# Performance work log

Hardware: AMD Instinct MI355X
Metric: run time of the kernel (lower is better)

Reference implementation:

```python
import jax, jax.numpy as jnp
import numpy as np
import math

D = 1024
H = 16
DH = D // H
FF = 4096
B, S = 2, 2048


def _layernorm(x, g, b, eps=1e-5):
    mu = jnp.mean(x, axis=-1, keepdims=True)
    var = jnp.var(x, axis=-1, keepdims=True)
    return (x - mu) * jax.lax.rsqrt(var + eps) * g + b


def _gelu_tanh(x):
    # 0.5*x*(1+tanh(sqrt(2/pi)*(x+0.044715*x^3)))
    c = math.sqrt(2.0 / math.pi)
    return 0.5 * x * (1.0 + jnp.tanh(c * (x + 0.044715 * x ** 3)))


def setup_inputs() -> dict:
    key = jax.random.key(0)
    ks = jax.random.split(key, 8)
    s = 0.02
    return {
        "x": jax.random.normal(ks[0], (B, S, D), dtype=jnp.float32),
        "ln1_g": jnp.ones((D,), jnp.float32),
        "ln1_b": jnp.zeros((D,), jnp.float32),
        "Wqkv": jax.random.normal(ks[1], (D, 3 * D), jnp.float32) * s,
        "bqkv": jnp.zeros((3 * D,), jnp.float32),
        "Wo": jax.random.normal(ks[2], (D, D), jnp.float32) * s,
        "bo": jnp.zeros((D,), jnp.float32),
        "ln2_g": jnp.ones((D,), jnp.float32),
        "ln2_b": jnp.zeros((D,), jnp.float32),
        "W1": jax.random.normal(ks[3], (D, FF), jnp.float32) * s,
        "b1": jnp.zeros((FF,), jnp.float32),
        "W2": jax.random.normal(ks[4], (FF, D), jnp.float32) * s,
        "b2": jnp.zeros((D,), jnp.float32),
    }


def reference(x, ln1_g, ln1_b, Wqkv, bqkv, Wo, bo, ln2_g, ln2_b, W1, b1, W2, b2):
    b, s, d = x.shape
    h = _layernorm(x, ln1_g, ln1_b)
    qkv = h @ Wqkv + bqkv                       # [B,S,3D]
    q, k, v = jnp.split(qkv, 3, axis=-1)
    q = q.reshape(b, s, H, DH).transpose(0, 2, 1, 3)   # [B,H,S,Dh]
    k = k.reshape(b, s, H, DH).transpose(0, 2, 1, 3)
    v = v.reshape(b, s, H, DH).transpose(0, 2, 1, 3)
    scores = jnp.einsum("bhqd,bhkd->bhqk", q, k) / math.sqrt(DH)
    probs = jax.nn.softmax(scores, axis=-1)
    attn = jnp.einsum("bhqk,bhkd->bhqd", probs, v)     # [B,H,S,Dh]
    attn = attn.transpose(0, 2, 1, 3).reshape(b, s, d)
    attn = attn @ Wo + bo
    x = x + attn
    m = _layernorm(x, ln2_g, ln2_b)
    m = _gelu_tanh(m @ W1 + b1) @ W2 + b2
    return x + m
```

## Files before the change

kernel.cpp:

```cpp
#include <hip/hip_runtime.h>
#include <hip/hip_bf16.h>
#include <cstdint>

#define D_ 1024
#define H_ 16
#define DH_ 64
#define FF_ 4096
#define B_ 2
#define S_ 2048
#define MR_ (B_ * S_)

typedef __bf16 bf16x8 __attribute__((ext_vector_type(8)));
typedef __bf16 bf16x4 __attribute__((ext_vector_type(4)));
typedef float f32x4 __attribute__((ext_vector_type(4)));
typedef float f32x16 __attribute__((ext_vector_type(16)));

__device__ __forceinline__ void g2lds16(const void* g, void* l) {
  __builtin_amdgcn_global_load_lds(
      (__attribute__((address_space(1))) void*)(uintptr_t)g,
      (__attribute__((address_space(3))) void*)(uint32_t)(uintptr_t)l,
      16, 0, 0);
}

__device__ __forceinline__ unsigned pkbf16(float lo, float hi) {
  unsigned r;
  asm("v_cvt_pk_bf16_f32 %0, %1, %2" : "=v"(r) : "v"(lo), "v"(hi));
  return r;
}

__device__ __forceinline__ float fexp2(float x) {
  return __builtin_amdgcn_exp2f(x);
}

__global__ __launch_bounds__(256) void transpose_cvt(
    const float* __restrict__ W, __hip_bfloat16* __restrict__ Wt, int K, int N) {
  __shared__ float t[32][33];
  int bx = blockIdx.x * 32;
  int by = blockIdx.y * 32;
  int tx = threadIdx.x, ty = threadIdx.y;
#pragma unroll
  for (int i = 0; i < 4; ++i)
    t[ty + 8 * i][tx] = W[(size_t)(by + ty + 8 * i) * N + bx + tx];
  __syncthreads();
#pragma unroll
  for (int i = 0; i < 4; ++i)
    Wt[(size_t)(bx + ty + 8 * i) * K + by + tx] = __float2bfloat16(t[tx][ty + 8 * i]);
}

__global__ __launch_bounds__(256) void transpose_v(
    const __hip_bfloat16* __restrict__ qkv, __hip_bfloat16* __restrict__ vT) {
  __shared__ __hip_bfloat16 t[32][33];
  int bh = blockIdx.z, b = bh >> 4, h = bh & 15;
  int s0 = blockIdx.x * 32, d0 = blockIdx.y * 32;
  int tx = threadIdx.x, ty = threadIdx.y;
#pragma unroll
  for (int i = 0; i < 4; ++i)
    t[ty + 8 * i][tx] =
        qkv[(size_t)(b * S_ + s0 + ty + 8 * i) * (3 * D_) + 2 * D_ + h * DH_ + d0 + tx];
  __syncthreads();
#pragma unroll
  for (int i = 0; i < 4; ++i)
    vT[(size_t)(bh * DH_ + d0 + ty + 8 * i) * S_ + s0 + tx] = t[tx][ty + 8 * i];
}

__global__ __launch_bounds__(256) void ln_kernel(
    const float* __restrict__ x, const float* __restrict__ g,
    const float* __restrict__ b, __hip_bfloat16* __restrict__ out) {
  int row = blockIdx.x;
  const float4* xr = (const float4*)(x + (size_t)row * D_);
  float4 v = xr[threadIdx.x];
  float s = v.x + v.y + v.z + v.w;
  float ss = v.x * v.x + v.y * v.y + v.z * v.z + v.w * v.w;
#pragma unroll
  for (int m = 1; m < 64; m <<= 1) {
    s += __shfl_xor(s, m);
    ss += __shfl_xor(ss, m);
  }
  __shared__ float rs[4], rss[4];
  int wave = threadIdx.x >> 6, lane = threadIdx.x & 63;
  if (lane == 0) { rs[wave] = s; rss[wave] = ss; }
  __syncthreads();
  s = rs[0] + rs[1] + rs[2] + rs[3];
  ss = rss[0] + rss[1] + rss[2] + rss[3];
  float mean = s * (1.0f / D_);
  float var = ss * (1.0f / D_) - mean * mean;
  float inv = rsqrtf(var + 1e-5f);
  int c = threadIdx.x * 4;
  float4 gv = ((const float4*)g)[threadIdx.x];
  float4 bv = ((const float4*)b)[threadIdx.x];
  __hip_bfloat16* o = out + (size_t)row * D_ + c;
  o[0] = __float2bfloat16((v.x - mean) * inv * gv.x + bv.x);
  o[1] = __float2bfloat16((v.y - mean) * inv * gv.y + bv.y);
  o[2] = __float2bfloat16((v.z - mean) * inv * gv.z + bv.z);
  o[3] = __float2bfloat16((v.w - mean) * inv * gv.w + bv.w);
}

template <int EPI>
__global__ __launch_bounds__(256) void gemm4(
    const __hip_bfloat16* __restrict__ A, const __hip_bfloat16* __restrict__ Bt,
    const float* __restrict__ bias, const float* __restrict__ resid,
    void* __restrict__ outp, int M, int N, int K) {
  constexpr int BM = 128, BN = 128, MF = 4, NF = 4;
  __shared__ alignas(16) __hip_bfloat16 sA[2][BM * 64];
  __shared__ alignas(16) __hip_bfloat16 sB[2][BN * 64];
  const int tid = threadIdx.x;
  const int lane = tid & 63, wave = tid >> 6;
  const int l15 = lane & 15, l4 = lane >> 4;
  const int wr = wave >> 1, wc = wave & 1;
  const int csw = (l15 & 7) << 3;

  const int gx = gridDim.x;
  int nwg = gx * gridDim.y;
  int flat = blockIdx.y * gx + blockIdx.x;
  int cpx = nwg >> 3;
  int swz = (flat & 7) * cpx + (flat >> 3);
  const int m0 = (swz / gx) * BM, n0 = (swz % gx) * BN;

  f32x4 z = {0.f, 0.f, 0.f, 0.f};
  f32x4 acc[MF][NF];
#pragma unroll
  for (int i = 0; i < MF; ++i)
#pragma unroll
    for (int j = 0; j < NF; ++j) acc[i][j] = z;

  auto stage = [&](int bu, int kt) {
#pragma unroll
    for (int it = 0; it < 4; ++it) {
      int idx = it * 256 + tid;
      int r = idx >> 3, c = (idx & 7) * 8;
      int cs = c ^ ((r & 7) << 3);
      g2lds16(A + (size_t)(m0 + r) * K + kt + cs, (void*)(&sA[bu][idx * 8]));
      g2lds16(Bt + (size_t)(n0 + r) * K + kt + cs, (void*)(&sB[bu][idx * 8]));
    }
  };

  const int nk = K / 64;
  stage(0, 0);
  asm volatile("s_waitcnt vmcnt(0)" ::: "memory");
  __builtin_amdgcn_s_barrier();

  for (int j = 0; j < nk; ++j) {
    const int cur = j & 1;
    if (j + 1 < nk) stage(cur ^ 1, (j + 1) * 64);

    __builtin_amdgcn_s_setprio(1);
#pragma unroll
    for (int kk = 0; kk < 2; ++kk) {
      int col = (kk * 32 + l4 * 8) ^ csw;
      bf16x8 bfr[NF];
#pragma unroll
      for (int nf = 0; nf < NF; ++nf)
        bfr[nf] = *(const bf16x8*)(&sB[cur][(wc * 64 + nf * 16 + l15) * 64 + col]);
#pragma unroll
      for (int mf = 0; mf < MF; ++mf) {
        bf16x8 af = *(const bf16x8*)(&sA[cur][(wr * 64 + mf * 16 + l15) * 64 + col]);
#pragma unroll
        for (int nf = 0; nf < NF; ++nf)
          acc[mf][nf] =
              __builtin_amdgcn_mfma_f32_16x16x32_bf16(af, bfr[nf], acc[mf][nf], 0, 0, 0);
      }
    }
    __builtin_amdgcn_s_setprio(0);

    asm volatile("s_waitcnt lgkmcnt(0)" ::: "memory");
    __builtin_amdgcn_sched_barrier(0);
    asm volatile("s_waitcnt vmcnt(0)" ::: "memory");
    __builtin_amdgcn_s_barrier();
    asm volatile("" ::: "memory");
  }

#pragma unroll
  for (int mf = 0; mf < MF; ++mf) {
#pragma unroll
    for (int nf = 0; nf < NF; ++nf) {
      int col = n0 + wc * 64 + nf * 16 + l15;
      float bv = bias[col];
#pragma unroll
      for (int j = 0; j < 4; ++j) {
        int row = m0 + wr * 64 + mf * 16 + l4 * 4 + j;
        size_t o = (size_t)row * N + col;
        float v = acc[mf][nf][j] + bv;
        if (EPI == 0) {
          ((__hip_bfloat16*)outp)[o] = __float2bfloat16(v);
        } else if (EPI == 1) {
          ((float*)outp)[o] = v + resid[o];
        } else {
          float a = 0.7978845608028654f * (v + 0.044715f * v * v * v);
          a = fminf(fmaxf(a, -15.f), 15.f);
          float e = __expf(2.f * a);
          float th = (e - 1.f) / (e + 1.f);
          ((__hip_bfloat16*)outp)[o] = __float2bfloat16(0.5f * v * (1.f + th));
        }
      }
    }
  }
}

template <int EPI>
__global__ __launch_bounds__(512) void gemmr3(
    const __hip_bfloat16* __restrict__ A, const __hip_bfloat16* __restrict__ Bt,
    const float* __restrict__ bias, const float* __restrict__ resid,
    void* __restrict__ outp, int M, int N, int K) {
  constexpr int BM = 128, BN = 128, MF = 4, NF = 2, WN = 4;
  __shared__ alignas(16) __hip_bfloat16 sA[3][BM * 64];
  __shared__ alignas(16) __hip_bfloat16 sB[3][BN * 64];
  const int tid = threadIdx.x;
  const int lane = tid & 63, wave = tid >> 6;
  const int l15 = lane & 15, l4 = lane >> 4;
  const int wr = wave / WN, wc = wave % WN;
  const int csw = (l15 & 7) << 3;

  const int gx = gridDim.x;
  int nwg = gx * gridDim.y;
  int flat = blockIdx.y * gx + blockIdx.x;
  int cpx = nwg >> 3;
  int swz = (flat & 7) * cpx + (flat >> 3);
  const int m0 = (swz / gx) * BM, n0 = (swz % gx) * BN;

  f32x4 z = {0.f, 0.f, 0.f, 0.f};
  f32x4 acc[MF][NF];
#pragma unroll
  for (int i = 0; i < MF; ++i)
#pragma unroll
    for (int j = 0; j < NF; ++j) acc[i][j] = z;

  auto stage = [&](int bu, int kt) {
#pragma unroll
    for (int it = 0; it < 2; ++it) {
      int idx = it * 512 + tid;
      int r = idx >> 3, c = (idx & 7) * 8;
      int cs = c ^ ((r & 7) << 3);
      g2lds16(A + (size_t)(m0 + r) * K + kt + cs, (void*)(&sA[bu][idx * 8]));
      g2lds16(Bt + (size_t)(n0 + r) * K + kt + cs, (void*)(&sB[bu][idx * 8]));
    }
  };

  const int nk = K / 64;
  stage(0, 0);
  stage(1, 64);
  asm volatile("s_waitcnt vmcnt(4)" ::: "memory");
  __builtin_amdgcn_s_barrier();

  int bu = 0, bu2 = 2;
  for (int j = 0; j < nk; ++j) {
    const bool pf = (j + 2) < nk;
    if (pf) stage(bu2, (j + 2) * 64);

    __builtin_amdgcn_s_setprio(1);
#pragma unroll
    for (int kk = 0; kk < 2; ++kk) {
      int col = (kk * 32 + l4 * 8) ^ csw;
      bf16x8 bfr[NF];
#pragma unroll
      for (int nf = 0; nf < NF; ++nf)
        bfr[nf] = *(const bf16x8*)(&sB[bu][(wc * NF * 16 + nf * 16 + l15) * 64 + col]);
#pragma unroll
      for (int mf = 0; mf < MF; ++mf) {
        bf16x8 af = *(const bf16x8*)(&sA[bu][(wr * MF * 16 + mf * 16 + l15) * 64 + col]);
#pragma unroll
        for (int nf = 0; nf < NF; ++nf)
          acc[mf][nf] =
              __builtin_amdgcn_mfma_f32_16x16x32_bf16(af, bfr[nf], acc[mf][nf], 0, 0, 0);
      }
    }
    __builtin_amdgcn_s_setprio(0);

    asm volatile("s_waitcnt lgkmcnt(0)" ::: "memory");
    __builtin_amdgcn_sched_barrier(0);
    if (pf)
      asm volatile("s_waitcnt vmcnt(4)" ::: "memory");
    else
      asm volatile("s_waitcnt vmcnt(0)" ::: "memory");
    __builtin_amdgcn_s_barrier();
    asm volatile("" ::: "memory");
    bu = (bu == 2) ? 0 : bu + 1;
    bu2 = (bu2 == 2) ? 0 : bu2 + 1;
  }

#pragma unroll
  for (int mf = 0; mf < MF; ++mf) {
#pragma unroll
    for (int nf = 0; nf < NF; ++nf) {
      int col = n0 + wc * NF * 16 + nf * 16 + l15;
      float bv = bias[col];
#pragma unroll
      for (int j = 0; j < 4; ++j) {
        int row = m0 + wr * MF * 16 + mf * 16 + l4 * 4 + j;
        size_t o = (size_t)row * N + col;
        float v = acc[mf][nf][j] + bv;
        if (EPI == 0) {
          ((__hip_bfloat16*)outp)[o] = __float2bfloat16(v);
        } else if (EPI == 1) {
          ((float*)outp)[o] = v + resid[o];
        } else {
          float a = 0.7978845608028654f * (v + 0.044715f * v * v * v);
          a = fminf(fmaxf(a, -15.f), 15.f);
          float e = __expf(2.f * a);
          float th = (e - 1.f) / (e + 1.f);
          ((__hip_bfloat16*)outp)[o] = __float2bfloat16(0.5f * v * (1.f + th));
        }
      }
    }
  }
}

__global__ __launch_bounds__(256) void attn_kernel(
    const __hip_bfloat16* __restrict__ qkv, const __hip_bfloat16* __restrict__ vT,
    __hip_bfloat16* __restrict__ out) {
  __shared__ alignas(16) __hip_bfloat16 sK[2][64 * 64];
  __shared__ alignas(16) __hip_bfloat16 sV[2][64 * 64];
  const int tid = threadIdx.x, lane = tid & 63, wave = tid >> 6;
  const int l31 = lane & 31, hi = lane >> 5;
  const int bh = blockIdx.y, b = bh >> 4, h = bh & 15;
  const int q0 = blockIdx.x * 128;
  const int rsw = (l31 & 7) << 3;
  const float k2 = 0.125f * 1.44269504f;

  bf16x8 qf[4];
  {
    int qr = q0 + wave * 32 + l31;
    const size_t qbase = ((size_t)(b * S_ + qr)) * (3 * D_) + h * DH_;
#pragma unroll
    for (int ks = 0; ks < 4; ++ks) {
      bf16x8 q = *(const bf16x8*)(qkv + qbase + ks * 16 + hi * 8);
#pragma unroll
      for (int i = 0; i < 8; ++i) q[i] = (__bf16)((float)q[i] * k2);
      qf[ks] = q;
    }
  }

  bf16x8 onesb;
#pragma unroll
  for (int i = 0; i < 8; ++i) onesb[i] = (__bf16)1.0f;

  f32x16 acc0, acc1, accL;
#pragma unroll
  for (int r = 0; r < 16; ++r) { acc0[r] = 0.f; acc1[r] = 0.f; accL[r] = 0.f; }

  const __hip_bfloat16* kg = qkv + (size_t)b * S_ * (3 * D_) + D_ + h * DH_;
  const __hip_bfloat16* vg = vT + (size_t)bh * DH_ * S_;

  auto stage = [&](int bu, int kv0) {
#pragma unroll
    for (int it = 0; it < 2; ++it) {
      int idx = it * 256 + tid;
      int r = idx >> 3;
      int c = (idx & 7) * 8;
      int cs = c ^ ((r & 7) << 3);
      g2lds16(kg + (size_t)(kv0 + r) * (3 * D_) + cs, (void*)(&sK[bu][idx * 8]));
      g2lds16(vg + (size_t)r * S_ + kv0 + cs, (void*)(&sV[bu][idx * 8]));
    }
  };

  stage(0, 0);
  const int NT = S_ / 64;

  for (int t = 0; t < NT; ++t) {
    const int cur = t & 1;
    __syncthreads();
    if (t + 1 < NT) stage(cur ^ 1, (t + 1) * 64);

    f32x16 sf0, sf1;
#pragma unroll
    for (int r = 0; r < 16; ++r) { sf0[r] = 0.f; sf1[r] = 0.f; }
    __builtin_amdgcn_s_setprio(1);
#pragma unroll
    for (int ks = 0; ks < 4; ++ks) {
      int colsw = (ks * 16 + hi * 8) ^ rsw;
      bf16x8 kf0 = *(const bf16x8*)(&sK[cur][l31 * 64 + colsw]);
      bf16x8 kf1 = *(const bf16x8*)(&sK[cur][(32 + l31) * 64 + colsw]);
      sf0 = __builtin_amdgcn_mfma_f32_32x32x16_bf16(kf0, qf[ks], sf0, 0, 0, 0);
      sf1 = __builtin_amdgcn_mfma_f32_32x32x16_bf16(kf1, qf[ks], sf1, 0, 0, 0);
    }
    __builtin_amdgcn_s_setprio(0);

    bf16x8 pa[4];
#pragma unroll
    for (int kb = 0; kb < 2; ++kb) {
      const f32x16 s16 = kb ? sf1 : sf0;
#pragma unroll
      for (int ksb = 0; ksb < 2; ++ksb) {
        float p0 = fexp2(s16[8 * ksb + 0]);
        float p1 = fexp2(s16[8 * ksb + 1]);
        float p2 = fexp2(s16[8 * ksb + 2]);
        float p3 = fexp2(s16[8 * ksb + 3]);
        float p4 = fexp2(s16[8 * ksb + 4]);
        float p5 = fexp2(s16[8 * ksb + 5]);
        float p6 = fexp2(s16[8 * ksb + 6]);
        float p7 = fexp2(s16[8 * ksb + 7]);
        unsigned wa = pkbf16(p0, p1), wb = pkbf16(p2, p3);
        unsigned wc = pkbf16(p4, p5), wd = pkbf16(p6, p7);
        auto r1 = __builtin_amdgcn_permlane32_swap(wa, wc, false, false);
        auto r2 = __builtin_amdgcn_permlane32_swap(wb, wd, false, false);
        union { unsigned u[4]; bf16x8 v; } w;
        w.u[0] = r1[0]; w.u[1] = r2[0]; w.u[2] = r1[1]; w.u[3] = r2[1];
        pa[kb * 2 + ksb] = w.v;
      }
    }

    __builtin_amdgcn_s_setprio(1);
#pragma unroll
    for (int ksg = 0; ksg < 4; ++ksg) {
      int colsw = (ksg * 16 + hi * 8) ^ rsw;
      bf16x8 vf0 = *(const bf16x8*)(&sV[cur][l31 * 64 + colsw]);
      bf16x8 vf1 = *(const bf16x8*)(&sV[cur][(32 + l31) * 64 + colsw]);
      acc0 = __builtin_amdgcn_mfma_f32_32x32x16_bf16(pa[ksg], vf0, acc0, 0, 0, 0);
      acc1 = __builtin_amdgcn_mfma_f32_32x32x16_bf16(pa[ksg], vf1, acc1, 0, 0, 0);
      accL = __builtin_amdgcn_mfma_f32_32x32x16_bf16(pa[ksg], onesb, accL, 0, 0, 0);
    }
    __builtin_amdgcn_s_setprio(0);
  }

#pragma unroll
  for (int r = 0; r < 16; ++r) {
    int qrow = (r & 3) + 8 * (r >> 2) + 4 * hi;
    float ir = 1.0f / accL[r];
    size_t obase = ((size_t)(b * S_ + q0 + wave * 32 + qrow)) * D_ + h * DH_ + l31;
    out[obase] = __float2bfloat16(acc0[r] * ir);
    out[obase + 32] = __float2bfloat16(acc1[r] * ir);
  }
}

extern "C" void kernel_launch(void* const* d_in, const int* in_sizes, int n_in,
                              void* d_out, int out_size, void* d_ws, size_t ws_size,
                              hipStream_t stream) {
  const float* x = (const float*)d_in[0];
  const float* ln1_g = (const float*)d_in[1];
  const float* ln1_b = (const float*)d_in[2];
  const float* Wqkv = (const float*)d_in[3];
  const float* bqkv = (const float*)d_in[4];
  const float* Wo = (const float*)d_in[5];
  const float* bo = (const float*)d_in[6];
  const float* ln2_g = (const float*)d_in[7];
  const float* ln2_b = (const float*)d_in[8];
  const float* W1 = (const float*)d_in[9];
  const float* b1 = (const float*)d_in[10];
  const float* W2 = (const float*)d_in[11];
  const float* b2 = (const float*)d_in[12];
  float* out = (float*)d_out;

  char* ws = (char*)d_ws;
  size_t off = 0;
  auto alloc = [&](size_t bytes) {
    void* p = ws + off;
    off += (bytes + 255) & ~(size_t)255;
    return p;
  };
  __hip_bfloat16* WqkvT = (__hip_bfloat16*)alloc((size_t)3 * D_ * D_ * 2);
  __hip_bfloat16* WoT = (__hip_bfloat16*)alloc((size_t)D_ * D_ * 2);
  __hip_bfloat16* W1T = (__hip_bfloat16*)alloc((size_t)FF_ * D_ * 2);
  __hip_bfloat16* W2T = (__hip_bfloat16*)alloc((size_t)D_ * FF_ * 2);
  __hip_bfloat16* h = (__hip_bfloat16*)alloc((size_t)MR_ * D_ * 2);
  __hip_bfloat16* qkv = (__hip_bfloat16*)alloc((size_t)MR_ * FF_ * 2);
  __hip_bfloat16* ff = qkv;
  __hip_bfloat16* vT = (__hip_bfloat16*)alloc((size_t)B_ * H_ * DH_ * S_ * 2);
  __hip_bfloat16* attn_out = (__hip_bfloat16*)alloc((size_t)MR_ * D_ * 2);

  dim3 tb(32, 8);
  transpose_cvt<<<dim3(3 * D_ / 32, D_ / 32), tb, 0, stream>>>(Wqkv, WqkvT, D_, 3 * D_);
  transpose_cvt<<<dim3(D_ / 32, D_ / 32), tb, 0, stream>>>(Wo, WoT, D_, D_);
  transpose_cvt<<<dim3(FF_ / 32, D_ / 32), tb, 0, stream>>>(W1, W1T, D_, FF_);
  transpose_cvt<<<dim3(D_ / 32, FF_ / 32), tb, 0, stream>>>(W2, W2T, FF_, D_);
  ln_kernel<<<MR_, 256, 0, stream>>>(x, ln1_g, ln1_b, h);
  gemm4<0><<<dim3(3 * D_ / 128, MR_ / 128), 256, 0, stream>>>(
      h, WqkvT, bqkv, nullptr, qkv, MR_, 3 * D_, D_);
  transpose_v<<<dim3(S_ / 32, DH_ / 32, B_ * H_), tb, 0, stream>>>(qkv, vT);
  attn_kernel<<<dim3(S_ / 128, B_ * H_), 256, 0, stream>>>(qkv, vT, attn_out);
  gemmr3<1><<<dim3(D_ / 128, MR_ / 128), 512, 0, stream>>>(
      attn_out, WoT, bo, x, out, MR_, D_, D_);
  ln_kernel<<<MR_, 256, 0, stream>>>(out, ln2_g, ln2_b, h);
  gemm4<2><<<dim3(FF_ / 128, MR_ / 128), 256, 0, stream>>>(
      h, W1T, b1, nullptr, ff, MR_, FF_, D_);
  gemmr3<1><<<dim3(D_ / 128, MR_ / 128), 512, 0, stream>>>(
      ff, W2T, b2, out, out, MR_, D_, FF_);
}
```

Baseline: 219.7 us.

## Process two 32-row query tiles per wave in attention to reuse K/V loads

Each wave in the attention kernel now handles 64 query rows, as two 32-row groups, instead of 32. Each K/V fragment read from LDS therefore feeds twice as many MFMAs, and each block stages K/V for 256 queries instead of 128, halving global K/V traffic. The cost is doubled accumulator and score registers, a hint of 2 blocks per CU, and half as many blocks (256 rather than 512). That reduces parallelism and may cause register spills.

```diff
diff --git a/kernel.cpp b/kernel.cpp
--- a/kernel.cpp
+++ b/kernel.cpp
@@ -304,7 +304,7 @@
   }
 }
 
-__global__ __launch_bounds__(256) void attn_kernel(
+__global__ __launch_bounds__(256, 2) void attn_kernel(
     const __hip_bfloat16* __restrict__ qkv, const __hip_bfloat16* __restrict__ vT,
     __hip_bfloat16* __restrict__ out) {
   __shared__ alignas(16) __hip_bfloat16 sK[2][64 * 64];
@@ -312,20 +312,26 @@
   const int tid = threadIdx.x, lane = tid & 63, wave = tid >> 6;
   const int l31 = lane & 31, hi = lane >> 5;
   const int bh = blockIdx.y, b = bh >> 4, h = bh & 15;
-  const int q0 = blockIdx.x * 128;
+  const int q0 = blockIdx.x * 256;
   const int rsw = (l31 & 7) << 3;
   const float k2 = 0.125f * 1.44269504f;
 
-  bf16x8 qf[4];
+  bf16x8 qfA[4], qfB[4];
   {
-    int qr = q0 + wave * 32 + l31;
-    const size_t qbase = ((size_t)(b * S_ + qr)) * (3 * D_) + h * DH_;
+    int qrA = q0 + wave * 64 + l31;
+    const size_t qbA = ((size_t)(b * S_ + qrA)) * (3 * D_) + h * DH_;
+    const size_t qbB = qbA + (size_t)32 * (3 * D_);
 #pragma unroll
     for (int ks = 0; ks < 4; ++ks) {
-      bf16x8 q = *(const bf16x8*)(qkv + qbase + ks * 16 + hi * 8);
-#pragma unroll
-      for (int i = 0; i < 8; ++i) q[i] = (__bf16)((float)q[i] * k2);
-      qf[ks] = q;
+      bf16x8 qa = *(const bf16x8*)(qkv + qbA + ks * 16 + hi * 8);
+      bf16x8 qb = *(const bf16x8*)(qkv + qbB + ks * 16 + hi * 8);
+#pragma unroll
+      for (int i = 0; i < 8; ++i) {
+        qa[i] = (__bf16)((float)qa[i] * k2);
+        qb[i] = (__bf16)((float)qb[i] * k2);
+      }
+      qfA[ks] = qa;
+      qfB[ks] = qb;
     }
   }
 
@@ -333,9 +339,12 @@
 #pragma unroll
   for (int i = 0; i < 8; ++i) onesb[i] = (__bf16)1.0f;
 
-  f32x16 acc0, acc1, accL;
-#pragma unroll
-  for (int r = 0; r < 16; ++r) { acc0[r] = 0.f; acc1[r] = 0.f; accL[r] = 0.f; }
+  f32x16 Z16;
+#pragma unroll
+  for (int r = 0; r < 16; ++r) Z16[r] = 0.f;
+
+  f32x16 accA0 = Z16, accA1 = Z16, accLA = Z16;
+  f32x16 accB0 = Z16, accB1 = Z16, accLB = Z16;
 
   const __hip_bfloat16* kg = qkv + (size_t)b * S_ * (3 * D_) + D_ + h * DH_;
   const __hip_bfloat16* vg = vT + (size_t)bh * DH_ * S_;
@@ -360,41 +369,56 @@
     __syncthreads();
     if (t + 1 < NT) stage(cur ^ 1, (t + 1) * 64);
 
-    f32x16 sf0, sf1;
-#pragma unroll
-    for (int r = 0; r < 16; ++r) { sf0[r] = 0.f; sf1[r] = 0.f; }
+    f32x16 sfA0, sfA1, sfB0, sfB1;
     __builtin_amdgcn_s_setprio(1);
-#pragma unroll
-    for (int ks = 0; ks < 4; ++ks) {
+    {
+      int colsw = (hi * 8) ^ rsw;
+      bf16x8 kf0 = *(const bf16x8*)(&sK[cur][l31 * 64 + colsw]);
+      bf16x8 kf1 = *(const bf16x8*)(&sK[cur][(32 + l31) * 64 + colsw]);
+      sfA0 = __builtin_amdgcn_mfma_f32_32x32x16_bf16(kf0, qfA[0], Z16, 0, 0, 0);
+      sfA1 = __builtin_amdgcn_mfma_f32_32x32x16_bf16(kf1, qfA[0], Z16, 0, 0, 0);
+      sfB0 = __builtin_amdgcn_mfma_f32_32x32x16_bf16(kf0, qfB[0], Z16, 0, 0, 0);
+      sfB1 = __builtin_amdgcn_mfma_f32_32x32x16_bf16(kf1, qfB[0], Z16, 0, 0, 0);
+    }
+#pragma unroll
+    for (int ks = 1; ks < 4; ++ks) {
       int colsw = (ks * 16 + hi * 8) ^ rsw;
       bf16x8 kf0 = *(const bf16x8*)(&sK[cur][l31 * 64 + colsw]);
       bf16x8 kf1 = *(const bf16x8*)(&sK[cur][(32 + l31) * 64 + colsw]);
-      sf0 = __builtin_amdgcn_mfma_f32_32x32x16_bf16(kf0, qf[ks], sf0, 0, 0, 0);
-      sf1 = __builtin_amdgcn_mfma_f32_32x32x16_bf16(kf1, qf[ks], sf1, 0, 0, 0);
+      sfA0 = __builtin_amdgcn_mfma_f32_32x32x16_bf16(kf0, qfA[ks], sfA0, 0, 0, 0);
+      sfA1 = __builtin_amdgcn_mfma_f32_32x32x16_bf16(kf1, qfA[ks], sfA1, 0, 0, 0);
+      sfB0 = __builtin_amdgcn_mfma_f32_32x32x16_bf16(kf0, qfB[ks], sfB0, 0, 0, 0);
+      sfB1 = __builtin_amdgcn_mfma_f32_32x32x16_bf16(kf1, qfB[ks], sfB1, 0, 0, 0);
     }
     __builtin_amdgcn_s_setprio(0);
 
-    bf16x8 pa[4];
-#pragma unroll
-    for (int kb = 0; kb < 2; ++kb) {
-      const f32x16 s16 = kb ? sf1 : sf0;
-#pragma unroll
-      for (int ksb = 0; ksb < 2; ++ksb) {
-        float p0 = fexp2(s16[8 * ksb + 0]);
-        float p1 = fexp2(s16[8 * ksb + 1]);
-        float p2 = fexp2(s16[8 * ksb + 2]);
-        float p3 = fexp2(s16[8 * ksb + 3]);
-        float p4 = fexp2(s16[8 * ksb + 4]);
-        float p5 = fexp2(s16[8 * ksb + 5]);
-        float p6 = fexp2(s16[8 * ksb + 6]);
-        float p7 = fexp2(s16[8 * ksb + 7]);
-        unsigned wa = pkbf16(p0, p1), wb = pkbf16(p2, p3);
-        unsigned wc = pkbf16(p4, p5), wd = pkbf16(p6, p7);
-        auto r1 = __builtin_amdgcn_permlane32_swap(wa, wc, false, false);
-        auto r2 = __builtin_amdgcn_permlane32_swap(wb, wd, false, false);
-        union { unsigned u[4]; bf16x8 v; } w;
-        w.u[0] = r1[0]; w.u[1] = r2[0]; w.u[2] = r1[1]; w.u[3] = r2[1];
-        pa[kb * 2 + ksb] = w.v;
+    bf16x8 paA[4], paB[4];
+#pragma unroll
+    for (int g = 0; g < 2; ++g) {
+      const f32x16& s0 = g ? sfB0 : sfA0;
+      const f32x16& s1 = g ? sfB1 : sfA1;
+      bf16x8* pa = g ? paB : paA;
+#pragma unroll
+      for (int kb = 0; kb < 2; ++kb) {
+        const f32x16& s16 = kb ? s1 : s0;
+#pragma unroll
+        for (int ksb = 0; ksb < 2; ++ksb) {
+          float p0 = fexp2(s16[8 * ksb + 0]);
+          float p1 = fexp2(s16[8 * ksb + 1]);
+          float p2 = fexp2(s16[8 * ksb + 2]);
+          float p3 = fexp2(s16[8 * ksb + 3]);
+          float p4 = fexp2(s16[8 * ksb + 4]);
+          float p5 = fexp2(s16[8 * ksb + 5]);
+          float p6 = fexp2(s16[8 * ksb + 6]);
+          float p7 = fexp2(s16[8 * ksb + 7]);
+          unsigned wa = pkbf16(p0, p1), wb = pkbf16(p2, p3);
+          unsigned wc = pkbf16(p4, p5), wd = pkbf16(p6, p7);
+          auto r1 = __builtin_amdgcn_permlane32_swap(wa, wc, false, false);
+          auto r2 = __builtin_amdgcn_permlane32_swap(wb, wd, false, false);
+          union { unsigned u[4]; bf16x8 v; } w;
+          w.u[0] = r1[0]; w.u[1] = r2[0]; w.u[2] = r1[1]; w.u[3] = r2[1];
+          pa[kb * 2 + ksb] = w.v;
+        }
       }
     }
 
@@ -404,9 +428,12 @@
       int colsw = (ksg * 16 + hi * 8) ^ rsw;
       bf16x8 vf0 = *(const bf16x8*)(&sV[cur][l31 * 64 + colsw]);
       bf16x8 vf1 = *(const bf16x8*)(&sV[cur][(32 + l31) * 64 + colsw]);
-      acc0 = __builtin_amdgcn_mfma_f32_32x32x16_bf16(pa[ksg], vf0, acc0, 0, 0, 0);
-      acc1 = __builtin_amdgcn_mfma_f32_32x32x16_bf16(pa[ksg], vf1, acc1, 0, 0, 0);
-      accL = __builtin_amdgcn_mfma_f32_32x32x16_bf16(pa[ksg], onesb, accL, 0, 0, 0);
+      accA0 = __builtin_amdgcn_mfma_f32_32x32x16_bf16(paA[ksg], vf0, accA0, 0, 0, 0);
+      accA1 = __builtin_amdgcn_mfma_f32_32x32x16_bf16(paA[ksg], vf1, accA1, 0, 0, 0);
+      accLA = __builtin_amdgcn_mfma_f32_32x32x16_bf16(paA[ksg], onesb, accLA, 0, 0, 0);
+      accB0 = __builtin_amdgcn_mfma_f32_32x32x16_bf16(paB[ksg], vf0, accB0, 0, 0, 0);
+      accB1 = __builtin_amdgcn_mfma_f32_32x32x16_bf16(paB[ksg], vf1, accB1, 0, 0, 0);
+      accLB = __builtin_amdgcn_mfma_f32_32x32x16_bf16(paB[ksg], onesb, accLB, 0, 0, 0);
     }
     __builtin_amdgcn_s_setprio(0);
   }
@@ -414,10 +441,14 @@
 #pragma unroll
   for (int r = 0; r < 16; ++r) {
     int qrow = (r & 3) + 8 * (r >> 2) + 4 * hi;
-    float ir = 1.0f / accL[r];
-    size_t obase = ((size_t)(b * S_ + q0 + wave * 32 + qrow)) * D_ + h * DH_ + l31;
-    out[obase] = __float2bfloat16(acc0[r] * ir);
-    out[obase + 32] = __float2bfloat16(acc1[r] * ir);
+    size_t obA = ((size_t)(b * S_ + q0 + wave * 64 + qrow)) * D_ + h * DH_ + l31;
+    size_t obB = obA + (size_t)32 * D_;
+    float irA = 1.0f / accLA[r];
+    float irB = 1.0f / accLB[r];
+    out[obA] = __float2bfloat16(accA0[r] * irA);
+    out[obA + 32] = __float2bfloat16(accA1[r] * irA);
+    out[obB] = __float2bfloat16(accB0[r] * irB);
+    out[obB + 32] = __float2bfloat16(accB1[r] * irB);
   }
 }
 
@@ -465,7 +496,7 @@
   gemm4<0><<<dim3(3 * D_ / 128, MR_ / 128), 256, 0, stream>>>(
       h, WqkvT, bqkv, nullptr, qkv, MR_, 3 * D_, D_);
   transpose_v<<<dim3(S_ / 32, DH_ / 32, B_ * H_), tb, 0, stream>>>(qkv, vT);
-  attn_kernel<<<dim3(S_ / 128, B_ * H_), 256, 0, stream>>>(qkv, vT, attn_out);
+  attn_kernel<<<dim3(S_ / 256, B_ * H_), 256, 0, stream>>>(qkv, vT, attn_out);
   gemmr3<1><<<dim3(D_ / 128, MR_ / 128), 512, 0, stream>>>(
       attn_out, WoT, bo, x, out, MR_, D_, D_);
   ln_kernel<<<MR_, 256, 0, stream>>>(out, ln2_g, ln2_b, h);
```

New measurement: 214.4 us. 1.02x faster.
